# Kernel optimization log

Measured on AMD Instinct MI355X. Metric: run time of the kernel, lower is better.

The kernel has to match this reference:

```python
import jax, jax.numpy as jnp
import numpy as np

IN_DIM = 256
OUT_DIM = 256
EMBED_DIM = 256
GROUPS = 8
BN_EPS = 1e-5


def conv2d(x, w, b, pad, groups=1):
    # x: NCHW, w: OIHW (I = in_ch / groups)
    out = jax.lax.conv_general_dilated(
        x, w, window_strides=(1, 1), padding=[(pad, pad), (pad, pad)],
        dimension_numbers=('NCHW', 'OIHW', 'NCHW'), feature_group_count=groups)
    return out + b[None, :, None, None]


def setup_inputs() -> dict:
    key = jax.random.key(0)
    ks = jax.random.split(key, 8)
    s = 0.05
    d = {}
    d['x'] = jax.random.normal(ks[0], (2, IN_DIM, 16, 16), jnp.float32)
    d['y'] = jax.random.normal(ks[1], (2, OUT_DIM, 128, 128), jnp.float32)
    # channle_reduce: Conv2d(256, 64, k=3, groups=64) -> weight (64, 4, 3, 3)
    d['w_cr'] = jax.random.normal(ks[2], (IN_DIM // 4, 4, 3, 3), jnp.float32) * s
    d['b_cr'] = jnp.zeros((IN_DIM // 4,), jnp.float32)
    # depthwise convs on 64 channels
    d['w_dw3'] = jax.random.normal(ks[3], (IN_DIM // 4, 1, 3, 3), jnp.float32) * s
    d['b_dw3'] = jnp.zeros((IN_DIM // 4,), jnp.float32)
    d['w_dw7'] = jax.random.normal(ks[4], (IN_DIM // 4, 1, 5, 5), jnp.float32) * s
    d['b_dw7'] = jnp.zeros((IN_DIM // 4,), jnp.float32)
    # gate: Conv2d(256, 128, 1) + BN + StarReLU
    d['w_gate'] = jax.random.normal(ks[5], (IN_DIM // 2, IN_DIM, 1, 1), jnp.float32) * s
    d['b_gate'] = jnp.zeros((IN_DIM // 2,), jnp.float32)
    d['bn_gamma'] = jnp.ones((IN_DIM // 2,), jnp.float32)
    d['bn_beta'] = jnp.zeros((IN_DIM // 2,), jnp.float32)
    d['bn_mean'] = jnp.zeros((IN_DIM // 2,), jnp.float32)
    d['bn_var'] = jnp.ones((IN_DIM // 2,), jnp.float32)
    d['sr_scale'] = jnp.ones((1,), jnp.float32)
    d['sr_bias'] = jnp.zeros((1,), jnp.float32)
    # linear1: Linear(16, 8192) -> torch weight shape (8192, 16)
    d['w_lin'] = jax.random.normal(ks[6], (OUT_DIM * EMBED_DIM // GROUPS, IN_DIM // (2 * GROUPS)), jnp.float32) * s
    d['b_lin'] = jnp.zeros((OUT_DIM * EMBED_DIM // GROUPS,), jnp.float32)
    return d


def reference(x, y, w_cr, b_cr, w_dw3, b_dw3, w_dw7, b_dw7, w_gate, b_gate,
              bn_gamma, bn_beta, bn_mean, bn_var, sr_scale, sr_bias, w_lin, b_lin):
    B, C, H, Wd = x.shape
    # gate branch: 1x1 conv -> BN (inference stats) -> StarReLU
    g = conv2d(x, w_gate, b_gate, 0)
    inv = (bn_gamma / jnp.sqrt(bn_var + BN_EPS))[None, :, None, None]
    g = (g - bn_mean[None, :, None, None]) * inv + bn_beta[None, :, None, None]
    g = sr_scale * jnp.square(jnp.maximum(g, 0.0)) + sr_bias
    # feature branch
    xr = conv2d(x, w_cr, b_cr, 1, groups=IN_DIM // 4)        # (B, 64, H, W)
    x3 = conv2d(xr, w_dw3, b_dw3, 1, groups=IN_DIM // 4)
    x7 = conv2d(xr, w_dw7, b_dw7, 2, groups=IN_DIM // 4)
    xc = jnp.concatenate([x3, x7], axis=1) * g               # (B, 128, H, W)
    # per-pixel weight generation: (B,H,W,G,16) @ (16,8192)
    xc = xc.reshape(B, GROUPS, -1, H, Wd).transpose(0, 3, 4, 1, 2)
    wdec = jnp.einsum('bhwgi,oi->bhwgo', xc, w_lin) + b_lin  # (B,H,W,8,8192)
    # flatten (G, out*embed/G) -> (embed, out); matches torch reshape order
    wdec = wdec.reshape(B, H, Wd, EMBED_DIM, OUT_DIM)
    # patch-wise dynamic 1x1 conv == per-patch batched matmul
    b, c, h, w = y.shape
    fh, fw = H, Wd
    ph, pw = h // fh, w // fw
    yp = y.reshape(b, c, fh, ph, fw, pw)
    # out[b,e,f,p,g,q] = sum_c wdec[b,f,g,e,c] * y[b,c,f,p,g,q]
    out = jnp.einsum('bfgec,bcfpgq->befpgq', wdec, yp)
    return out.reshape(b, EMBED_DIM, h, w)
```

## Files before the change

kernel.cpp:

```cpp
#include <hip/hip_runtime.h>
#include <stdint.h>


typedef __attribute__((ext_vector_type(8))) short short8;
typedef __attribute__((ext_vector_type(4))) float f32x4;

#define BN_EPS 1e-5f

__device__ __forceinline__ unsigned short f2bf(float f) {
  unsigned u = __float_as_uint(f);
  return (unsigned short)((u + 0x8000u) >> 16);
}
__device__ __forceinline__ unsigned pk2bf(float a, float b) {
  unsigned ua = __float_as_uint(a), ub = __float_as_uint(b);
  return ((ua + 0x8000u) >> 16) | ((ub + 0x8000u) & 0xFFFF0000u);
}

__global__ __launch_bounds__(256) void k1_merged(
    const float* __restrict__ x, const float* __restrict__ w_cr,
    const float* __restrict__ b_cr, const float* __restrict__ w_dw3,
    const float* __restrict__ b_dw3, const float* __restrict__ w_dw7,
    const float* __restrict__ b_dw7, const float* __restrict__ w_gate,
    const float* __restrict__ b_gate, const float* __restrict__ bn_gamma,
    const float* __restrict__ bn_beta, const float* __restrict__ bn_mean,
    const float* __restrict__ bn_var, const float* __restrict__ sr_scale,
    const float* __restrict__ sr_bias, const float* __restrict__ w_lin,
    short* __restrict__ wlin_bf, float* __restrict__ f0_out,
    float* __restrict__ gs_out)
{
  __shared__ __align__(16) float xcen[256];
  __shared__ __align__(16) float xs[4][256];
  __shared__ __align__(16) float xrs[256];

  int blk = blockIdx.x;
  int t = threadIdx.x;

  if (blk < 512) {
    int b = blk >> 8, h = (blk >> 4) & 15, w = blk & 15;
    int pix = (b * 16 + h) * 16 + w;

    { int idx = blk * 256 + t; wlin_bf[idx] = (short)f2bf(w_lin[idx]); }

    xcen[t] = x[b * 65536 + t * 256 + h * 16 + w];
    __syncthreads();

    int wave = t >> 6, lane = t & 63;
    int oq = lane >> 2, ol = lane & 3;
    const float4* wg4 = (const float4*)w_gate;
    const float4* xc4 = (const float4*)xcen;
    float ss = sr_scale[0], sb = sr_bias[0];

    #pragma unroll
    for (int pass = 0; pass < 2; ++pass) {
      int o = wave * 32 + pass * 16 + oq;
      float acc = 0.f;
      #pragma unroll
      for (int k = 0; k < 16; ++k) {
        int j = k * 4 + ol;
        float4 wv = wg4[o * 64 + j];
        float4 xv = xc4[j];
        acc += wv.x * xv.x + wv.y * xv.y + wv.z * xv.z + wv.w * xv.w;
      }
      acc += __shfl_xor(acc, 1);
      acc += __shfl_xor(acc, 2);
      float inv = bn_gamma[o] * rsqrtf(bn_var[o] + BN_EPS);
      float gg = (acc + b_gate[o] - bn_mean[o]) * inv + bn_beta[o];
      gg = fmaxf(gg, 0.f);
      gg = ss * gg * gg + sb;
      if (ol == 0) gs_out[pix * 128 + o] = gg;
    }
  } else {
    int cb = blk - 512;
    int b = cb >> 6, cr = cb & 63;
    {
      int ch = t >> 6, off = (t & 63) * 4;
      float4 v = *(const float4*)(x + b * 65536 + (cr * 4 + ch) * 256 + off);
      *(float4*)&xs[ch][off] = v;
    }
    __syncthreads();
    int h = t >> 4, w = t & 15;
    float a = b_cr[cr];
    #pragma unroll
    for (int ii = 0; ii < 4; ++ii) {
      const float* wp = w_cr + (cr * 4 + ii) * 9;
      #pragma unroll
      for (int ky = 0; ky < 3; ++ky) {
        int gy = h + ky - 1;
        #pragma unroll
        for (int kx = 0; kx < 3; ++kx) {
          int gx = w + kx - 1;
          float v = (gy >= 0 && gy < 16 && gx >= 0 && gx < 16) ? xs[ii][gy * 16 + gx] : 0.f;
          a += wp[ky * 3 + kx] * v;
        }
      }
    }
    xrs[t] = a;
    __syncthreads();

    float f3 = b_dw3[cr];
    {
      const float* wp = w_dw3 + cr * 9;
      #pragma unroll
      for (int ky = 0; ky < 3; ++ky) {
        int gy = h + ky - 1;
        #pragma unroll
        for (int kx = 0; kx < 3; ++kx) {
          int gx = w + kx - 1;
          float v = (gy >= 0 && gy < 16 && gx >= 0 && gx < 16) ? xrs[gy * 16 + gx] : 0.f;
          f3 += wp[ky * 3 + kx] * v;
        }
      }
    }
    float f5 = b_dw7[cr];
    {
      const float* wp = w_dw7 + cr * 25;
      #pragma unroll
      for (int ky = 0; ky < 5; ++ky) {
        int gy = h + ky - 2;
        #pragma unroll
        for (int kx = 0; kx < 5; ++kx) {
          int gx = w + kx - 2;
          float v = (gy >= 0 && gy < 16 && gx >= 0 && gx < 16) ? xrs[gy * 16 + gx] : 0.f;
          f5 += wp[ky * 5 + kx] * v;
        }
      }
    }
    int pix = (b * 16 + h) * 16 + w;
    f0_out[pix * 128 + cr] = f3;
    f0_out[pix * 128 + 64 + cr] = f5;
  }
}

__global__ __launch_bounds__(512, 6) void k2_fused(
    const float* __restrict__ y, const short* __restrict__ wlin_bf,
    const float* __restrict__ f0_in, const float* __restrict__ gs_in,
    const float* __restrict__ b_lin, float* __restrict__ out)
{
  __shared__ __align__(16) short Ylds[16384];
  __shared__ __align__(16) char dyn[16384];
  float* scratch = (float*)dyn;
  short* wdbuf = (short*)dyn;

  int phys = blockIdx.x;
  int logical = (phys & 7) * 128 + (phys >> 3);
  int patch = logical >> 1, ehalf = logical & 1;
  int b = patch >> 8, f = (patch >> 4) & 15, g = patch & 15;
  int gbase = ehalf * 4;
  int tid = threadIdx.x;
  int wave = tid >> 6, lane = tid & 63;
  int quad = lane >> 4, l16 = lane & 15;

  const float* yb = y + b * 4194304 + (f * 8) * 128 + g * 8;

  int c32 = tid >> 4, pf = tid & 15;
  for (int sch = 0; sch < 4; ++sch) {
    float4 v[2];
    #pragma unroll
    for (int it = 0; it < 2; ++it)
      v[it] = *(const float4*)(yb + (sch * 64 + it * 32 + c32) * 16384 + (pf >> 1) * 128 + (pf & 1) * 4);
    #pragma unroll
    for (int it = 0; it < 2; ++it)
      *(float4*)&scratch[(it * 32 + c32) * 64 + pf * 4] = v[it];
    __syncthreads();
    {
      int pix = tid & 63, cg = tid >> 6;
      float s0 = scratch[(cg * 8 + 0) * 64 + pix];
      float s1 = scratch[(cg * 8 + 1) * 64 + pix];
      float s2 = scratch[(cg * 8 + 2) * 64 + pix];
      float s3 = scratch[(cg * 8 + 3) * 64 + pix];
      float s4 = scratch[(cg * 8 + 4) * 64 + pix];
      float s5 = scratch[(cg * 8 + 5) * 64 + pix];
      float s6 = scratch[(cg * 8 + 6) * 64 + pix];
      float s7 = scratch[(cg * 8 + 7) * 64 + pix];
      uint4 pk;
      pk.x = pk2bf(s0, s1); pk.y = pk2bf(s2, s3);
      pk.z = pk2bf(s4, s5); pk.w = pk2bf(s6, s7);
      int chunk = sch * 8 + cg;
      int physc = chunk ^ (pix & 7);
      *(uint4*)&Ylds[pix * 256 + physc * 8] = pk;
    }
    __syncthreads();
  }

  int geff = l16 & 7, jsel = l16 >> 3;
  bool bvalid = (geff < 4) && (jsel == (quad >> 1));
  short8 bx = {0, 0, 0, 0, 0, 0, 0, 0};
  if (bvalid) {
    const float* fp = f0_in + patch * 128 + (gbase + geff) * 16 + (quad & 1) * 8;
    const float* gp = gs_in + patch * 128 + (gbase + geff) * 16 + (quad & 1) * 8;
    float4 fa = *(const float4*)fp, fb = *(const float4*)(fp + 4);
    float4 ga = *(const float4*)gp, gb = *(const float4*)(gp + 4);
    bx[0] = (short)f2bf(fa.x * ga.x); bx[1] = (short)f2bf(fa.y * ga.y);
    bx[2] = (short)f2bf(fa.z * ga.z); bx[3] = (short)f2bf(fa.w * ga.w);
    bx[4] = (short)f2bf(fb.x * gb.x); bx[5] = (short)f2bf(fb.y * gb.y);
    bx[6] = (short)f2bf(fb.z * gb.z); bx[7] = (short)f2bf(fb.w * gb.w);
  }

  f32x4 zero4 = {0.f, 0.f, 0.f, 0.f};
  f32x4 acc[4];
  #pragma unroll
  for (int nt = 0; nt < 4; ++nt) acc[nt] = zero4;

  int jA_half = quad >> 1;
  auto gen_chunk = [&](int cc, int buf) {
    short* dst = wdbuf + buf * 4096;
    #pragma unroll
    for (int jj = 0; jj < 2; ++jj) {
      int jp = wave * 2 + jj;
      int jA = jp * 2 + jA_half;
      int jD = jp * 2 + jsel;
      #pragma unroll
      for (int hh = 0; hh < 2; ++hh) {
        int c0 = cc * 32 + hh * 16;
        short8 aw = *(const short8*)(wlin_bf + (jA * 256 + c0 + l16) * 16 + (quad & 1) * 8);
        f32x4 d = __builtin_amdgcn_mfma_f32_16x16x32_bf16(aw, bx, zero4, 0, 0, 0);
        if (geff < 4) {
          int e = geff * 32 + jD;
          float4 bl = *(const float4*)(b_lin + jD * 256 + c0 + quad * 4);
          uint2 pk;
          pk.x = pk2bf(d[0] + bl.x, d[1] + bl.y);
          pk.y = pk2bf(d[2] + bl.z, d[3] + bl.w);
          int q16 = hh * 2 + (quad >> 1);
          int sw = q16 ^ ((e >> 1) & 3) ^ ((e >> 5) & 3);
          *(uint2*)&dst[e * 32 + sw * 8 + (quad & 1) * 4] = pk;
        }
      }
    }
  };

  gen_chunk(0, 0);
  __syncthreads();

  for (int cc = 0; cc < 8; ++cc) {
    if (cc < 7) gen_chunk(cc + 1, (cc + 1) & 1);

    const short* src = wdbuf + (cc & 1) * 4096;
    short8 A2, Bf[4];
    {
      int e = wave * 16 + l16;
      int sw = quad ^ ((e >> 1) & 3) ^ ((e >> 5) & 3);
      A2 = *(const short8*)&src[e * 32 + sw * 8];
    }
    int chunkY = cc * 4 + quad;
    #pragma unroll
    for (int nt = 0; nt < 4; ++nt) {
      int nn = nt * 16 + l16;
      int physc = chunkY ^ (nn & 7);
      Bf[nt] = *(const short8*)&Ylds[nn * 256 + physc * 8];
    }
    #pragma unroll
    for (int nt = 0; nt < 4; ++nt)
      acc[nt] = __builtin_amdgcn_mfma_f32_16x16x32_bf16(A2, Bf[nt], acc[nt], 0, 0, 0);
    __syncthreads();
  }

  float* ob = out + b * 4194304 + (f * 8) * 128 + g * 8;
  int e0 = ehalf * 128 + wave * 16 + quad * 4;
  #pragma unroll
  for (int nt = 0; nt < 4; ++nt) {
    int pix = nt * 16 + l16;
    float* oa = ob + (pix >> 3) * 128 + (pix & 7);
    #pragma unroll
    for (int r = 0; r < 4; ++r)
      oa[(e0 + r) * 16384] = acc[nt][r];
  }
}

extern "C" void kernel_launch(void* const* d_in, const int* in_sizes, int n_in,
                              void* d_out, int out_size, void* d_ws, size_t ws_size,
                              hipStream_t stream) {
  const float* x        = (const float*)d_in[0];
  const float* y        = (const float*)d_in[1];
  const float* w_cr     = (const float*)d_in[2];
  const float* b_cr     = (const float*)d_in[3];
  const float* w_dw3    = (const float*)d_in[4];
  const float* b_dw3    = (const float*)d_in[5];
  const float* w_dw7    = (const float*)d_in[6];
  const float* b_dw7    = (const float*)d_in[7];
  const float* w_gate   = (const float*)d_in[8];
  const float* b_gate   = (const float*)d_in[9];
  const float* bn_gamma = (const float*)d_in[10];
  const float* bn_beta  = (const float*)d_in[11];
  const float* bn_mean  = (const float*)d_in[12];
  const float* bn_var   = (const float*)d_in[13];
  const float* sr_scale = (const float*)d_in[14];
  const float* sr_bias  = (const float*)d_in[15];
  const float* w_lin    = (const float*)d_in[16];
  const float* b_lin    = (const float*)d_in[17];
  float* out = (float*)d_out;

  float* f0      = (float*)d_ws;
  float* gs      = (float*)((char*)d_ws + 262144);
  short* wlin_bf = (short*)((char*)d_ws + 524288);

  hipLaunchKernelGGL(k1_merged, dim3(640), dim3(256), 0, stream,
                     x, w_cr, b_cr, w_dw3, b_dw3, w_dw7, b_dw7, w_gate, b_gate,
                     bn_gamma, bn_beta, bn_mean, bn_var, sr_scale, sr_bias,
                     w_lin, wlin_bf, f0, gs);
  hipLaunchKernelGGL(k2_fused, dim3(1024), dim3(512), 0, stream,
                     y, wlin_bf, f0, gs, b_lin, out);
}
```

Before: 167.6 us.

## Process full embed dim per block, prefetch y and weights into registers

Each block now handles all 256 output embeddings for a patch instead of half, halving the grid and removing the duplicated y load and bf16 transpose per patch. The kernel prefetches all y tiles and the next linear-weight fragments into registers before use, folds the bias into the MFMA accumulator input, pads the scratch transpose stride to 65, and widens the LDS swizzle. The cost is double-sized weight buffers in LDS, more registers, lower occupancy (launch bounds 6 to 4), and only 512 blocks to spread across CUs.

```diff
diff --git a/kernel.cpp b/kernel.cpp
--- a/kernel.cpp
+++ b/kernel.cpp
@@ -131,138 +131,169 @@
   }
 }
 
-__global__ __launch_bounds__(512, 6) void k2_fused(
+__global__ __launch_bounds__(512, 4) void k2_fused(
     const float* __restrict__ y, const short* __restrict__ wlin_bf,
     const float* __restrict__ f0_in, const float* __restrict__ gs_in,
     const float* __restrict__ b_lin, float* __restrict__ out)
 {
   __shared__ __align__(16) short Ylds[16384];
-  __shared__ __align__(16) char dyn[16384];
+  __shared__ __align__(16) char dyn[32768];
   float* scratch = (float*)dyn;
   short* wdbuf = (short*)dyn;
 
   int phys = blockIdx.x;
-  int logical = (phys & 7) * 128 + (phys >> 3);
-  int patch = logical >> 1, ehalf = logical & 1;
-  int b = patch >> 8, f = (patch >> 4) & 15, g = patch & 15;
-  int gbase = ehalf * 4;
+  int blk = (phys & 7) * 64 + (phys >> 3);
+  int b = blk >> 8, f = (blk >> 4) & 15, g = blk & 15;
   int tid = threadIdx.x;
   int wave = tid >> 6, lane = tid & 63;
   int quad = lane >> 4, l16 = lane & 15;
+  int geff = l16 & 7, jsel = l16 >> 3;
 
   const float* yb = y + b * 4194304 + (f * 8) * 128 + g * 8;
 
   int c32 = tid >> 4, pf = tid & 15;
+  float4 yv[4][2];
+  #pragma unroll
+  for (int sch = 0; sch < 4; ++sch)
+    #pragma unroll
+    for (int it = 0; it < 2; ++it)
+      yv[sch][it] = *(const float4*)(yb + (sch * 64 + it * 32 + c32) * 16384 + (pf >> 1) * 128 + (pf & 1) * 4);
+
+  short8 aw[2][2][2];
+  #pragma unroll
+  for (int s = 0; s < 2; ++s)
+    #pragma unroll
+    for (int jj = 0; jj < 2; ++jj) {
+      int jA = (wave * 2 + jj) * 2 + (quad >> 1);
+      #pragma unroll
+      for (int hh = 0; hh < 2; ++hh) {
+        int c0 = s * 32 + hh * 16;
+        aw[s][jj][hh] = *(const short8*)(wlin_bf + (jA * 256 + c0 + l16) * 16 + (quad & 1) * 8);
+      }
+    }
+
+  bool bval = (jsel == (quad >> 1));
+  const float* fp = f0_in + blk * 128 + geff * 16 + (quad & 1) * 8;
+  const float* gp = gs_in + blk * 128 + geff * 16 + (quad & 1) * 8;
+  float4 f0a = *(const float4*)fp, f0b = *(const float4*)(fp + 4);
+  float4 gsa = *(const float4*)gp, gsb = *(const float4*)(gp + 4);
+
+  #pragma unroll
   for (int sch = 0; sch < 4; ++sch) {
-    float4 v[2];
     #pragma unroll
     for (int it = 0; it < 2; ++it)
-      v[it] = *(const float4*)(yb + (sch * 64 + it * 32 + c32) * 16384 + (pf >> 1) * 128 + (pf & 1) * 4);
-    #pragma unroll
-    for (int it = 0; it < 2; ++it)
-      *(float4*)&scratch[(it * 32 + c32) * 64 + pf * 4] = v[it];
+      *(float4*)&scratch[(it * 32 + c32) * 65 + pf * 4] = yv[sch][it];
     __syncthreads();
     {
       int pix = tid & 63, cg = tid >> 6;
-      float s0 = scratch[(cg * 8 + 0) * 64 + pix];
-      float s1 = scratch[(cg * 8 + 1) * 64 + pix];
-      float s2 = scratch[(cg * 8 + 2) * 64 + pix];
-      float s3 = scratch[(cg * 8 + 3) * 64 + pix];
-      float s4 = scratch[(cg * 8 + 4) * 64 + pix];
-      float s5 = scratch[(cg * 8 + 5) * 64 + pix];
-      float s6 = scratch[(cg * 8 + 6) * 64 + pix];
-      float s7 = scratch[(cg * 8 + 7) * 64 + pix];
+      float s0 = scratch[(cg * 8 + 0) * 65 + pix];
+      float s1 = scratch[(cg * 8 + 1) * 65 + pix];
+      float s2 = scratch[(cg * 8 + 2) * 65 + pix];
+      float s3 = scratch[(cg * 8 + 3) * 65 + pix];
+      float s4 = scratch[(cg * 8 + 4) * 65 + pix];
+      float s5 = scratch[(cg * 8 + 5) * 65 + pix];
+      float s6 = scratch[(cg * 8 + 6) * 65 + pix];
+      float s7 = scratch[(cg * 8 + 7) * 65 + pix];
       uint4 pk;
       pk.x = pk2bf(s0, s1); pk.y = pk2bf(s2, s3);
       pk.z = pk2bf(s4, s5); pk.w = pk2bf(s6, s7);
       int chunk = sch * 8 + cg;
-      int physc = chunk ^ (pix & 7);
+      int physc = chunk ^ (pix & 15);
       *(uint4*)&Ylds[pix * 256 + physc * 8] = pk;
     }
     __syncthreads();
   }
 
-  int geff = l16 & 7, jsel = l16 >> 3;
-  bool bvalid = (geff < 4) && (jsel == (quad >> 1));
   short8 bx = {0, 0, 0, 0, 0, 0, 0, 0};
-  if (bvalid) {
-    const float* fp = f0_in + patch * 128 + (gbase + geff) * 16 + (quad & 1) * 8;
-    const float* gp = gs_in + patch * 128 + (gbase + geff) * 16 + (quad & 1) * 8;
-    float4 fa = *(const float4*)fp, fb = *(const float4*)(fp + 4);
-    float4 ga = *(const float4*)gp, gb = *(const float4*)(gp + 4);
-    bx[0] = (short)f2bf(fa.x * ga.x); bx[1] = (short)f2bf(fa.y * ga.y);
-    bx[2] = (short)f2bf(fa.z * ga.z); bx[3] = (short)f2bf(fa.w * ga.w);
-    bx[4] = (short)f2bf(fb.x * gb.x); bx[5] = (short)f2bf(fb.y * gb.y);
-    bx[6] = (short)f2bf(fb.z * gb.z); bx[7] = (short)f2bf(fb.w * gb.w);
-  }
-
-  f32x4 zero4 = {0.f, 0.f, 0.f, 0.f};
-  f32x4 acc[4];
-  #pragma unroll
-  for (int nt = 0; nt < 4; ++nt) acc[nt] = zero4;
-
-  int jA_half = quad >> 1;
-  auto gen_chunk = [&](int cc, int buf) {
-    short* dst = wdbuf + buf * 4096;
+  if (bval) {
+    bx[0] = (short)f2bf(f0a.x * gsa.x); bx[1] = (short)f2bf(f0a.y * gsa.y);
+    bx[2] = (short)f2bf(f0a.z * gsa.z); bx[3] = (short)f2bf(f0a.w * gsa.w);
+    bx[4] = (short)f2bf(f0b.x * gsb.x); bx[5] = (short)f2bf(f0b.y * gsb.y);
+    bx[6] = (short)f2bf(f0b.z * gsb.z); bx[7] = (short)f2bf(f0b.w * gsb.w);
+  }
+
+  f32x4 acc[2][4];
+  #pragma unroll
+  for (int et = 0; et < 2; ++et)
+    #pragma unroll
+    for (int nt = 0; nt < 4; ++nt)
+      acc[et][nt] = {0.f, 0.f, 0.f, 0.f};
+
+  auto gen_chunk = [&](int cc, int buf, int slot) {
+    short* dst = wdbuf + buf * 8192;
     #pragma unroll
     for (int jj = 0; jj < 2; ++jj) {
       int jp = wave * 2 + jj;
-      int jA = jp * 2 + jA_half;
       int jD = jp * 2 + jsel;
       #pragma unroll
       for (int hh = 0; hh < 2; ++hh) {
         int c0 = cc * 32 + hh * 16;
-        short8 aw = *(const short8*)(wlin_bf + (jA * 256 + c0 + l16) * 16 + (quad & 1) * 8);
-        f32x4 d = __builtin_amdgcn_mfma_f32_16x16x32_bf16(aw, bx, zero4, 0, 0, 0);
-        if (geff < 4) {
-          int e = geff * 32 + jD;
-          float4 bl = *(const float4*)(b_lin + jD * 256 + c0 + quad * 4);
-          uint2 pk;
-          pk.x = pk2bf(d[0] + bl.x, d[1] + bl.y);
-          pk.y = pk2bf(d[2] + bl.z, d[3] + bl.w);
-          int q16 = hh * 2 + (quad >> 1);
-          int sw = q16 ^ ((e >> 1) & 3) ^ ((e >> 5) & 3);
-          *(uint2*)&dst[e * 32 + sw * 8 + (quad & 1) * 4] = pk;
+        float4 bl = *(const float4*)(b_lin + jD * 256 + c0 + quad * 4);
+        f32x4 cin = {bl.x, bl.y, bl.z, bl.w};
+        f32x4 d = __builtin_amdgcn_mfma_f32_16x16x32_bf16(aw[slot][jj][hh], bx, cin, 0, 0, 0);
+        int e = geff * 32 + jD;
+        uint2 pk;
+        pk.x = pk2bf(d[0], d[1]);
+        pk.y = pk2bf(d[2], d[3]);
+        int q16 = hh * 2 + (quad >> 1);
+        int sw = q16 ^ ((e >> 1) & 3) ^ ((e >> 5) & 3);
+        *(uint2*)&dst[e * 32 + sw * 8 + (quad & 1) * 4] = pk;
+      }
+    }
+  };
+
+  gen_chunk(0, 0, 0);
+  __syncthreads();
+
+  #pragma unroll
+  for (int cc = 0; cc < 8; ++cc) {
+    if (cc < 6) {
+      #pragma unroll
+      for (int jj = 0; jj < 2; ++jj) {
+        int jA = (wave * 2 + jj) * 2 + (quad >> 1);
+        #pragma unroll
+        for (int hh = 0; hh < 2; ++hh) {
+          int c0 = (cc + 2) * 32 + hh * 16;
+          aw[cc & 1][jj][hh] = *(const short8*)(wlin_bf + (jA * 256 + c0 + l16) * 16 + (quad & 1) * 8);
         }
       }
     }
-  };
-
-  gen_chunk(0, 0);
-  __syncthreads();
-
-  for (int cc = 0; cc < 8; ++cc) {
-    if (cc < 7) gen_chunk(cc + 1, (cc + 1) & 1);
-
-    const short* src = wdbuf + (cc & 1) * 4096;
-    short8 A2, Bf[4];
-    {
-      int e = wave * 16 + l16;
+    if (cc < 7) gen_chunk(cc + 1, (cc + 1) & 1, (cc + 1) & 1);
+
+    const short* src = wdbuf + (cc & 1) * 8192;
+    short8 A2[2], Bf[4];
+    #pragma unroll
+    for (int et = 0; et < 2; ++et) {
+      int e = wave * 32 + et * 16 + l16;
       int sw = quad ^ ((e >> 1) & 3) ^ ((e >> 5) & 3);
-      A2 = *(const short8*)&src[e * 32 + sw * 8];
+      A2[et] = *(const short8*)&src[e * 32 + sw * 8];
     }
     int chunkY = cc * 4 + quad;
     #pragma unroll
     for (int nt = 0; nt < 4; ++nt) {
-      int nn = nt * 16 + l16;
-      int physc = chunkY ^ (nn & 7);
-      Bf[nt] = *(const short8*)&Ylds[nn * 256 + physc * 8];
-    }
-    #pragma unroll
-    for (int nt = 0; nt < 4; ++nt)
-      acc[nt] = __builtin_amdgcn_mfma_f32_16x16x32_bf16(A2, Bf[nt], acc[nt], 0, 0, 0);
-    __syncthreads();
+      int physc = chunkY ^ l16;
+      Bf[nt] = *(const short8*)&Ylds[(nt * 16 + l16) * 256 + physc * 8];
+    }
+    #pragma unroll
+    for (int et = 0; et < 2; ++et)
+      #pragma unroll
+      for (int nt = 0; nt < 4; ++nt)
+        acc[et][nt] = __builtin_amdgcn_mfma_f32_16x16x32_bf16(A2[et], Bf[nt], acc[et][nt], 0, 0, 0);
+    if (cc < 7) __syncthreads();
   }
 
   float* ob = out + b * 4194304 + (f * 8) * 128 + g * 8;
-  int e0 = ehalf * 128 + wave * 16 + quad * 4;
-  #pragma unroll
-  for (int nt = 0; nt < 4; ++nt) {
-    int pix = nt * 16 + l16;
-    float* oa = ob + (pix >> 3) * 128 + (pix & 7);
-    #pragma unroll
-    for (int r = 0; r < 4; ++r)
-      oa[(e0 + r) * 16384] = acc[nt][r];
+  #pragma unroll
+  for (int et = 0; et < 2; ++et) {
+    int e0 = wave * 32 + et * 16 + quad * 4;
+    #pragma unroll
+    for (int nt = 0; nt < 4; ++nt) {
+      int pix = nt * 16 + l16;
+      float* oa = ob + (pix >> 3) * 128 + (pix & 7);
+      #pragma unroll
+      for (int r = 0; r < 4; ++r)
+        oa[(e0 + r) * 16384] = acc[et][nt][r];
+    }
   }
 }
 
@@ -297,6 +328,6 @@
                      x, w_cr, b_cr, w_dw3, b_dw3, w_dw7, b_dw7, w_gate, b_gate,
                      bn_gamma, bn_beta, bn_mean, bn_var, sr_scale, sr_bias,
                      w_lin, wlin_bf, f0, gs);
-  hipLaunchKernelGGL(k2_fused, dim3(1024), dim3(512), 0, stream,
+  hipLaunchKernelGGL(k2_fused, dim3(512), dim3(512), 0, stream,
                      y, wlin_bf, f0, gs, b_lin, out);
 }
```

After: 153.0 us. 1.1x faster.
